# Optimization experiments

Hardware: AMD Instinct MI355X
Metric: run time of the kernel (lower is better)

Reference implementation:

```python
import jax, jax.numpy as jnp
import numpy as np

BN_EPS = 1e-5

def _bn_relu(x, gamma, beta, mean, var):
    # x: [B, N, C]; BatchNorm1d(N) in eval mode normalizes over dim=1 (N)
    inv = jax.lax.rsqrt(var + BN_EPS)
    scale = (gamma * inv)[None, :, None]
    shift = (beta - mean * gamma * inv)[None, :, None]
    return jax.nn.relu(x * scale + shift)

def _forward(x, q_gamma, q_beta, q_mean, q_var,
             k_gamma, k_beta, k_mean, k_var,
             v_gamma, v_beta, v_mean, v_var,
             Wq, Wk, Wv, Wp):
    B, C, H, W = x.shape
    N = H * W
    E = Wq.shape[0]
    xs = x.reshape(B, C, N).transpose(0, 2, 1)  # [B, N, C]
    # BN+ReLU over spatial axis, then Linear(N->E) on spatial axis per channel -> [B, E, C]
    q = jnp.einsum('bnc,en->bec', _bn_relu(xs, q_gamma, q_beta, q_mean, q_var), Wq)
    k = jnp.einsum('bnc,en->bec', _bn_relu(xs, k_gamma, k_beta, k_mean, k_var), Wk)
    v = jnp.einsum('bnc,en->bec', _bn_relu(xs, v_gamma, v_beta, v_mean, v_var), Wv)
    scores = jnp.einsum('bec,bfc->bef', q, k) / jnp.sqrt(jnp.asarray(E, x.dtype))  # [B, E, E]
    attn = jax.nn.softmax(scores, axis=-1)
    out = jnp.einsum('bef,bfc->bec', attn, v)          # [B, E, C]
    out = jnp.einsum('bec,ne->bcn', out, Wp)            # Linear(E->N) -> [B, C, N]
    return out.reshape(B, C, H, W)

def setup_inputs() -> dict:
    key = jax.random.key(0)
    ks = jax.random.split(key, 20)
    B, C, H, W = 32, 512, 32, 32
    N = H * W  # sp_dim = 1024
    E = 1024   # embed_dim
    d = {'x': jax.random.normal(ks[0], (B, C, H, W), jnp.float32)}
    i = 1
    for p in ('q', 'k', 'v'):
        d[f'{p}_gamma'] = jax.random.uniform(ks[i], (N,), jnp.float32, 0.5, 1.5); i += 1
        d[f'{p}_beta'] = 0.1 * jax.random.normal(ks[i], (N,), jnp.float32); i += 1
        d[f'{p}_mean'] = 0.1 * jax.random.normal(ks[i], (N,), jnp.float32); i += 1
        d[f'{p}_var'] = jax.random.uniform(ks[i], (N,), jnp.float32, 0.5, 1.5); i += 1
    # torch Linear weight layout: [out, in]; scale ~ 1/sqrt(fan_in)
    d['Wq'] = jax.random.normal(ks[i], (E, N), jnp.float32) * (1.0 / np.sqrt(N)); i += 1
    d['Wk'] = jax.random.normal(ks[i], (E, N), jnp.float32) * (1.0 / np.sqrt(N)); i += 1
    d['Wv'] = jax.random.normal(ks[i], (E, N), jnp.float32) * (1.0 / np.sqrt(N)); i += 1
    d['Wp'] = jax.random.normal(ks[i], (N, E), jnp.float32) * (1.0 / np.sqrt(E)); i += 1
    return d

def reference(x, q_gamma, q_beta, q_mean, q_var,
              k_gamma, k_beta, k_mean, k_var,
              v_gamma, v_beta, v_mean, v_var,
              Wq, Wk, Wv, Wp):
    return _forward(x, q_gamma, q_beta, q_mean, q_var,
                    k_gamma, k_beta, k_mean, k_var,
                    v_gamma, v_beta, v_mean, v_var,
                    Wq, Wk, Wv, Wp)
```

## Files before the change

### kernel.cpp

```cpp
#include <hip/hip_runtime.h>
#include <math.h>

#define BN_EPS 1e-5f

namespace {

constexpr int Bb = 32;
constexpr int Cc = 512;
constexpr int Nn = 1024;
constexpr int Ee = 1024;

typedef __attribute__((ext_vector_type(8))) short short8;
typedef __attribute__((ext_vector_type(4))) float f32x4;
typedef __attribute__((ext_vector_type(4))) unsigned short ushort4_t;

struct bfpair { unsigned short h, l; };

__device__ __forceinline__ unsigned short bf16_rne(float v) {
  unsigned u = __builtin_bit_cast(unsigned, v);
  unsigned r = u + 0x7FFFu + ((u >> 16) & 1u);
  return (unsigned short)(r >> 16);
}
__device__ __forceinline__ float bf16_to_f(unsigned short h) {
  unsigned u = ((unsigned)h) << 16;
  return __builtin_bit_cast(float, u);
}
__device__ __forceinline__ bfpair split_bf(float v) {
  bfpair p;
  p.h = bf16_rne(v);
  p.l = bf16_rne(v - bf16_to_f(p.h));
  return p;
}

__device__ __forceinline__ void gll16(const void* g, void* l) {
  __builtin_amdgcn_global_load_lds(
      (const __attribute__((address_space(1))) void*)g,
      (__attribute__((address_space(3))) void*)l, 16, 0, 0);
}

__global__ __launch_bounds__(256) void prep_st_kernel(
    const float* __restrict__ g, const float* __restrict__ be,
    const float* __restrict__ mn, const float* __restrict__ vr,
    float* __restrict__ s, float* __restrict__ t, int n) {
  int i = blockIdx.x * blockDim.x + threadIdx.x;
  if (i < n) {
    float inv = rsqrtf(vr[i] + BN_EPS);
    float sc = g[i] * inv;
    s[i] = sc;
    t[i] = be[i] - mn[i] * sc;
  }
}

__global__ __launch_bounds__(256) void convert_y(
    const float* __restrict__ x, const float* __restrict__ s, const float* __restrict__ tt,
    unsigned short* __restrict__ yh, unsigned short* __restrict__ yl, long total4) {
  for (long i = (long)blockIdx.x * 256 + threadIdx.x; i < total4; i += (long)gridDim.x * 256) {
    float4 v = ((const float4*)x)[i];
    int n4 = (int)(i & 255);
    float4 s4 = ((const float4*)s)[n4];
    float4 t4 = ((const float4*)tt)[n4];
    float e0 = fmaxf(fmaf(v.x, s4.x, t4.x), 0.f);
    float e1 = fmaxf(fmaf(v.y, s4.y, t4.y), 0.f);
    float e2 = fmaxf(fmaf(v.z, s4.z, t4.z), 0.f);
    float e3 = fmaxf(fmaf(v.w, s4.w, t4.w), 0.f);
    bfpair p0 = split_bf(e0), p1 = split_bf(e1), p2 = split_bf(e2), p3 = split_bf(e3);
    ushort4_t hv, lv;
    hv.x = p0.h; hv.y = p1.h; hv.z = p2.h; hv.w = p3.h;
    lv.x = p0.l; lv.y = p1.l; lv.z = p2.l; lv.w = p3.l;
    *(ushort4_t*)&yh[i * 4] = hv;
    *(ushort4_t*)&yl[i * 4] = lv;
  }
}

__global__ __launch_bounds__(256) void convert_w(
    const float* __restrict__ wsrc, unsigned short* __restrict__ wh,
    unsigned short* __restrict__ wl, long total4) {
  for (long i = (long)blockIdx.x * 256 + threadIdx.x; i < total4; i += (long)gridDim.x * 256) {
    float4 v = ((const float4*)wsrc)[i];
    bfpair p0 = split_bf(v.x), p1 = split_bf(v.y), p2 = split_bf(v.z), p3 = split_bf(v.w);
    ushort4_t hv, lv;
    hv.x = p0.h; hv.y = p1.h; hv.z = p2.h; hv.w = p3.h;
    lv.x = p0.l; lv.y = p1.l; lv.z = p2.l; lv.w = p3.l;
    *(ushort4_t*)&wh[i * 4] = hv;
    *(ushort4_t*)&wl[i * 4] = lv;
  }
}

template<bool SPLIT>
__global__ __launch_bounds__(256) void gemm3(
    const unsigned short* __restrict__ Ah, const unsigned short* __restrict__ Al,
    long ldA, long bsA,
    const unsigned short* __restrict__ Bh, const unsigned short* __restrict__ Bl,
    long ldB, long bsB,
    float* __restrict__ Cf, unsigned short* __restrict__ Chi, unsigned short* __restrict__ Clo,
    long ldC, long bsC, int K, float alpha) {
  __shared__ unsigned short sAh[128][32], sAl[128][32], sBh[128][32], sBl[128][32];

  const int t = threadIdx.x, lane = t & 63, w = t >> 6;
  const int m0 = blockIdx.y * 128, n0 = blockIdx.x * 128;
  const long zb = blockIdx.z;

  const int sr = lane >> 2;
  const int sk = (lane & 3) * 8;
  const int wr = w >> 1, wc = w & 1;
  const int fr = lane & 15;
  const int kq = (lane >> 4) * 8;

  const unsigned short* a0 = Ah + zb * bsA + (long)(m0 + w * 32 + sr) * ldA + sk;
  const unsigned short* a1 = Al + zb * bsA + (long)(m0 + w * 32 + sr) * ldA + sk;
  const unsigned short* b0 = Bh + zb * bsB + (long)(n0 + w * 32 + sr) * ldB + sk;
  const unsigned short* b1 = Bl + zb * bsB + (long)(n0 + w * 32 + sr) * ldB + sk;
  const long a16 = 16 * ldA, b16 = 16 * ldB;

  f32x4 acc[4][4] = {};

  for (int k0 = 0; k0 < K; k0 += 32) {
    __syncthreads();
    gll16(a0, &sAh[w * 32][0]);      gll16(a0 + a16, &sAh[w * 32 + 16][0]);
    gll16(a1, &sAl[w * 32][0]);      gll16(a1 + a16, &sAl[w * 32 + 16][0]);
    gll16(b0, &sBh[w * 32][0]);      gll16(b0 + b16, &sBh[w * 32 + 16][0]);
    gll16(b1, &sBl[w * 32][0]);      gll16(b1 + b16, &sBl[w * 32 + 16][0]);
    a0 += 32; a1 += 32; b0 += 32; b1 += 32;
    __syncthreads();

    short8 ah[4], al[4], bh[4], bl[4];
#pragma unroll
    for (int i = 0; i < 4; ++i) {
      ah[i] = *(const short8*)&sAh[wr * 64 + i * 16 + fr][kq];
      al[i] = *(const short8*)&sAl[wr * 64 + i * 16 + fr][kq];
      bh[i] = *(const short8*)&sBh[wc * 64 + i * 16 + fr][kq];
      bl[i] = *(const short8*)&sBl[wc * 64 + i * 16 + fr][kq];
    }
#pragma unroll
    for (int i = 0; i < 4; ++i)
#pragma unroll
      for (int j = 0; j < 4; ++j) {
        acc[i][j] = __builtin_amdgcn_mfma_f32_16x16x32_bf16(ah[i], bh[j], acc[i][j], 0, 0, 0);
        acc[i][j] = __builtin_amdgcn_mfma_f32_16x16x32_bf16(ah[i], bl[j], acc[i][j], 0, 0, 0);
        acc[i][j] = __builtin_amdgcn_mfma_f32_16x16x32_bf16(al[i], bh[j], acc[i][j], 0, 0, 0);
      }
  }

  const int rb = (lane >> 4) * 4;
#pragma unroll
  for (int i = 0; i < 4; ++i)
#pragma unroll
    for (int j = 0; j < 4; ++j) {
      long col = n0 + wc * 64 + j * 16 + fr;
#pragma unroll
      for (int v = 0; v < 4; ++v) {
        long row = m0 + wr * 64 + i * 16 + rb + v;
        float val = acc[i][j][v] * alpha;
        long idx = zb * bsC + row * ldC + col;
        if (SPLIT) {
          bfpair p = split_bf(val);
          Chi[idx] = p.h;
          Clo[idx] = p.l;
        } else {
          Cf[idx] = val;
        }
      }
    }
}

__global__ __launch_bounds__(256) void softmax_rows(float* __restrict__ S) {
  long row = blockIdx.x;
  float* p = S + row * 1024;
  int t = threadIdx.x;
  float4 v = *(float4*)(p + 4 * t);
  float mx = fmaxf(fmaxf(v.x, v.y), fmaxf(v.z, v.w));
#pragma unroll
  for (int i = 1; i < 64; i <<= 1) mx = fmaxf(mx, __shfl_xor(mx, i));
  __shared__ float redm[4];
  __shared__ float reds[4];
  int wave = t >> 6, lane = t & 63;
  if (lane == 0) redm[wave] = mx;
  __syncthreads();
  mx = fmaxf(fmaxf(redm[0], redm[1]), fmaxf(redm[2], redm[3]));
  float e0 = expf(v.x - mx), e1 = expf(v.y - mx);
  float e2 = expf(v.z - mx), e3 = expf(v.w - mx);
  float sum = (e0 + e1) + (e2 + e3);
#pragma unroll
  for (int i = 1; i < 64; i <<= 1) sum += __shfl_xor(sum, i);
  if (lane == 0) reds[wave] = sum;
  __syncthreads();
  sum = (reds[0] + reds[1]) + (reds[2] + reds[3]);
  float inv = 1.0f / sum;
  bfpair p0 = split_bf(e0 * inv), p1 = split_bf(e1 * inv);
  bfpair p2 = split_bf(e2 * inv), p3 = split_bf(e3 * inv);
  ushort4_t hv, lv;
  hv.x = p0.h; hv.y = p1.h; hv.z = p2.h; hv.w = p3.h;
  lv.x = p0.l; lv.y = p1.l; lv.z = p2.l; lv.w = p3.l;
  unsigned short* ph = (unsigned short*)p;
  *(ushort4_t*)&ph[4 * t] = hv;
  *(ushort4_t*)&ph[1024 + 4 * t] = lv;
}

}

extern "C" void kernel_launch(void* const* d_in, const int* in_sizes, int n_in,
                              void* d_out, int out_size, void* d_ws, size_t ws_size,
                              hipStream_t stream) {
  const float* x  = (const float*)d_in[0];
  const float* qg = (const float*)d_in[1];
  const float* qb = (const float*)d_in[2];
  const float* qm = (const float*)d_in[3];
  const float* qv = (const float*)d_in[4];
  const float* kg = (const float*)d_in[5];
  const float* kb = (const float*)d_in[6];
  const float* km = (const float*)d_in[7];
  const float* kv = (const float*)d_in[8];
  const float* vg = (const float*)d_in[9];
  const float* vb = (const float*)d_in[10];
  const float* vm = (const float*)d_in[11];
  const float* vv = (const float*)d_in[12];
  const float* Wq = (const float*)d_in[13];
  const float* Wk = (const float*)d_in[14];
  const float* Wv = (const float*)d_in[15];
  const float* Wp = (const float*)d_in[16];

  const size_t wMB = 8UL * 1024 * 1024 * 2;
  const size_t perB = 12UL * 1024 * 1024;
  int G = 32;
  while (G > 1 && 65536 + wMB + (size_t)G * perB > ws_size) G >>= 1;

  char* ws = (char*)d_ws;
  float* sq = (float*)ws;
  float* tq = sq + 1024;
  float* sk = tq + 1024;
  float* tk = sk + 1024;
  float* sv = tk + 1024;
  float* tv = sv + 1024;

  const long WE = 1024L * 1024;
  unsigned short* Wqh = (unsigned short*)(ws + 65536);
  unsigned short* Wql = Wqh + WE;
  unsigned short* Wkh = Wql + WE;
  unsigned short* Wkl = Wkh + WE;
  unsigned short* Wvh = Wkl + WE;
  unsigned short* Wvl = Wvh + WE;
  unsigned short* Wph = Wvl + WE;
  unsigned short* Wpl = Wph + WE;

  const long PB = (long)Cc * Ee;
  unsigned short* yh  = Wpl + WE;
  unsigned short* yl  = yh + (long)G * PB;
  unsigned short* Qh  = yl + (long)G * PB;
  unsigned short* Ql  = Qh + (long)G * PB;
  unsigned short* Kh  = Ql + (long)G * PB;
  unsigned short* Kl  = Kh + (long)G * PB;
  unsigned short* Vth = Kl + (long)G * PB;
  unsigned short* Vtl = Vth + (long)G * PB;
  float* S = (float*)(Vtl + (long)G * PB);
  unsigned short* Oth = Qh;
  unsigned short* Otl = Ql;

  dim3 blk(256);

  prep_st_kernel<<<dim3(4), blk, 0, stream>>>(qg, qb, qm, qv, sq, tq, Nn);
  prep_st_kernel<<<dim3(4), blk, 0, stream>>>(kg, kb, km, kv, sk, tk, Nn);
  prep_st_kernel<<<dim3(4), blk, 0, stream>>>(vg, vb, vm, vv, sv, tv, Nn);

  const long W4 = WE / 4;
  convert_w<<<dim3(1024), blk, 0, stream>>>(Wq, Wqh, Wql, W4);
  convert_w<<<dim3(1024), blk, 0, stream>>>(Wk, Wkh, Wkl, W4);
  convert_w<<<dim3(1024), blk, 0, stream>>>(Wv, Wvh, Wvl, W4);
  convert_w<<<dim3(1024), blk, 0, stream>>>(Wp, Wph, Wpl, W4);

  const long y4 = (long)G * PB / 4;

  for (int b0 = 0; b0 < Bb; b0 += G) {
    const float* xg = x + (size_t)b0 * Cc * Nn;
    float* outg = (float*)d_out + (size_t)b0 * Cc * Nn;

    convert_y<<<dim3(2048), blk, 0, stream>>>(xg, sq, tq, yh, yl, y4);
    gemm3<true><<<dim3(Cc / 128, Ee / 128, G), blk, 0, stream>>>(
        Wqh, Wql, Nn, 0L, yh, yl, Nn, PB,
        nullptr, Qh, Ql, Cc, PB, Nn, 1.0f);
    convert_y<<<dim3(2048), blk, 0, stream>>>(xg, sk, tk, yh, yl, y4);
    gemm3<true><<<dim3(Cc / 128, Ee / 128, G), blk, 0, stream>>>(
        Wkh, Wkl, Nn, 0L, yh, yl, Nn, PB,
        nullptr, Kh, Kl, Cc, PB, Nn, 1.0f);
    convert_y<<<dim3(2048), blk, 0, stream>>>(xg, sv, tv, yh, yl, y4);
    gemm3<true><<<dim3(Ee / 128, Cc / 128, G), blk, 0, stream>>>(
        yh, yl, Nn, PB, Wvh, Wvl, Nn, 0L,
        nullptr, Vth, Vtl, Ee, PB, Nn, 1.0f);
    gemm3<false><<<dim3(Ee / 128, Ee / 128, G), blk, 0, stream>>>(
        Qh, Ql, Cc, PB, Kh, Kl, Cc, PB,
        S, nullptr, nullptr, Ee, (long)Ee * Ee, Cc, 0.03125f);
    softmax_rows<<<dim3(G * Ee), blk, 0, stream>>>(S);
    gemm3<true><<<dim3(Ee / 128, Cc / 128, G), blk, 0, stream>>>(
        Vth, Vtl, Ee, PB, (unsigned short*)S, (unsigned short*)S + 1024,
        2L * Ee, 2L * Ee * Ee,
        nullptr, Oth, Otl, Ee, PB, Ee, 1.0f);
    gemm3<false><<<dim3(Nn / 128, Cc / 128, G), blk, 0, stream>>>(
        Oth, Otl, Ee, PB, Wph, Wpl, Ee, 0L,
        outg, nullptr, nullptr, Nn, (long)Cc * Nn, Ee, 1.0f);
  }
}
```

Before: 865.5 us.

## Fuse BN+ReLU+split into projection GEMMs, merge Q/K GEMM, swizzle LDS

Replaces the separate convert_y passes with a gemm_bn kernel that loads fp32 activations, applies BN+ReLU, splits them into bf16 hi/lo pairs and writes them straight to LDS inside the GEMM mainloop. Q and K projections are merged into one GEMM over a stacked 2048-row weight, and V is computed once for all batches into the output buffer as scratch. The change also adds XOR swizzling of LDS columns, a flattened 1D grid with block remapping, and fused prep of the three BN scale/shift vectors. The aim is to cut the intermediate bf16 activation traffic and launch count; in exchange the activation conversion is done with register loads in the GEMM, and the output buffer is reused for V, which relies on the P·V step reading each batch's V before the final projection overwrites it.

```diff
diff --git a/kernel.cpp b/kernel.cpp
--- a/kernel.cpp
+++ b/kernel.cpp
@@ -38,37 +38,23 @@
       (__attribute__((address_space(3))) void*)l, 16, 0, 0);
 }
 
-__global__ __launch_bounds__(256) void prep_st_kernel(
-    const float* __restrict__ g, const float* __restrict__ be,
-    const float* __restrict__ mn, const float* __restrict__ vr,
-    float* __restrict__ s, float* __restrict__ t, int n) {
+__global__ __launch_bounds__(256) void prep3(
+    const float* __restrict__ qg, const float* __restrict__ qb,
+    const float* __restrict__ qm, const float* __restrict__ qv,
+    const float* __restrict__ kg, const float* __restrict__ kb,
+    const float* __restrict__ km, const float* __restrict__ kv,
+    const float* __restrict__ vg, const float* __restrict__ vb,
+    const float* __restrict__ vm, const float* __restrict__ vv,
+    float* __restrict__ hdr) {
   int i = blockIdx.x * blockDim.x + threadIdx.x;
-  if (i < n) {
-    float inv = rsqrtf(vr[i] + BN_EPS);
-    float sc = g[i] * inv;
-    s[i] = sc;
-    t[i] = be[i] - mn[i] * sc;
-  }
-}
-
-__global__ __launch_bounds__(256) void convert_y(
-    const float* __restrict__ x, const float* __restrict__ s, const float* __restrict__ tt,
-    unsigned short* __restrict__ yh, unsigned short* __restrict__ yl, long total4) {
-  for (long i = (long)blockIdx.x * 256 + threadIdx.x; i < total4; i += (long)gridDim.x * 256) {
-    float4 v = ((const float4*)x)[i];
-    int n4 = (int)(i & 255);
-    float4 s4 = ((const float4*)s)[n4];
-    float4 t4 = ((const float4*)tt)[n4];
-    float e0 = fmaxf(fmaf(v.x, s4.x, t4.x), 0.f);
-    float e1 = fmaxf(fmaf(v.y, s4.y, t4.y), 0.f);
-    float e2 = fmaxf(fmaf(v.z, s4.z, t4.z), 0.f);
-    float e3 = fmaxf(fmaf(v.w, s4.w, t4.w), 0.f);
-    bfpair p0 = split_bf(e0), p1 = split_bf(e1), p2 = split_bf(e2), p3 = split_bf(e3);
-    ushort4_t hv, lv;
-    hv.x = p0.h; hv.y = p1.h; hv.z = p2.h; hv.w = p3.h;
-    lv.x = p0.l; lv.y = p1.l; lv.z = p2.l; lv.w = p3.l;
-    *(ushort4_t*)&yh[i * 4] = hv;
-    *(ushort4_t*)&yl[i * 4] = lv;
+  if (i < 1024) {
+    float inv, sc;
+    inv = rsqrtf(qv[i] + BN_EPS); sc = qg[i] * inv;
+    hdr[i] = sc;          hdr[1024 + i] = qb[i] - qm[i] * sc;
+    inv = rsqrtf(kv[i] + BN_EPS); sc = kg[i] * inv;
+    hdr[2048 + i] = sc;   hdr[3072 + i] = kb[i] - km[i] * sc;
+    inv = rsqrtf(vv[i] + BN_EPS); sc = vg[i] * inv;
+    hdr[4096 + i] = sc;   hdr[5120 + i] = vb[i] - vm[i] * sc;
   }
 }
 
@@ -86,6 +72,124 @@
   }
 }
 
+
+template<bool BN_ON_A, bool MFIRST>
+__global__ __launch_bounds__(256) void gemm_bn(
+    const unsigned short* __restrict__ Wh, const unsigned short* __restrict__ Wl,
+    const float* __restrict__ X, long bsX,
+    const float* __restrict__ s0, const float* __restrict__ t0,
+    const float* __restrict__ s1, const float* __restrict__ t1,
+    unsigned short* __restrict__ Chi, unsigned short* __restrict__ Clo,
+    long ldC, long bsC, int g0, int g1) {
+  constexpr int K = 1024;
+  __shared__ unsigned short sWh[128][32], sWl[128][32], sXh[128][32], sXl[128][32];
+
+  const int nb = gridDim.x;
+  int f = blockIdx.x;
+  if ((nb & 7) == 0) f = (f & 7) * (nb >> 3) + (f >> 3);
+  const int i0 = f % g0, i1 = (f / g0) % g1;
+  const long zb = f / (g0 * g1);
+  const int m0 = (MFIRST ? i0 : i1) * 128;
+  const int n0 = (MFIRST ? i1 : i0) * 128;
+
+  const int t = threadIdx.x, lane = t & 63, w = t >> 6;
+  const int sr  = lane >> 2;
+  const int skc = (((lane & 3) ^ ((lane >> 3) & 3)) * 8);
+  const int wr = w >> 1, wc = w & 1;
+  const int fr = lane & 15;
+  const int kq = ((((lane >> 4) & 3) ^ ((fr >> 1) & 3)) * 8);
+
+  const float* sb = s0;
+  const float* tb = t0;
+  if (!BN_ON_A && m0 >= 1024) { sb = s1; tb = t1; }
+
+  const int wrow0 = BN_ON_A ? n0 : m0;
+  const unsigned short* w0 = Wh + (long)(wrow0 + w * 32 + sr) * K + skc;
+  const unsigned short* w1 = Wl + (long)(wrow0 + w * 32 + sr) * K + skc;
+  const long w16 = 16L * K;
+
+  const int xrow0 = BN_ON_A ? m0 : n0;
+  const int xr = t >> 1, xh = t & 1;
+  const float* xp = X + zb * bsX + (long)(xrow0 + xr) * Nn + xh * 16;
+  const int swzr = (xr >> 1) & 3;
+
+  typedef unsigned short (*tile_t)[32];
+  tile_t pA0 = BN_ON_A ? sXh : sWh;
+  tile_t pA1 = BN_ON_A ? sXl : sWl;
+  tile_t pB0 = BN_ON_A ? sWh : sXh;
+  tile_t pB1 = BN_ON_A ? sWl : sXl;
+
+  f32x4 acc[4][4] = {};
+
+  for (int k0 = 0; k0 < K; k0 += 32) {
+    float4 xv[4];
+#pragma unroll
+    for (int j = 0; j < 4; ++j) xv[j] = *(const float4*)(xp + k0 + 4 * j);
+
+    __syncthreads();
+    gll16(w0, &sWh[w * 32][0]);  gll16(w0 + w16, &sWh[w * 32 + 16][0]);
+    gll16(w1, &sWl[w * 32][0]);  gll16(w1 + w16, &sWl[w * 32 + 16][0]);
+    w0 += 32; w1 += 32;
+
+    const int kbase = k0 + xh * 16;
+#pragma unroll
+    for (int cc = 0; cc < 2; ++cc) {
+      short8 hv, lv;
+#pragma unroll
+      for (int j = 0; j < 2; ++j) {
+        float4 v  = xv[cc * 2 + j];
+        float4 s4 = *(const float4*)(sb + kbase + cc * 8 + j * 4);
+        float4 t4 = *(const float4*)(tb + kbase + cc * 8 + j * 4);
+        bfpair p0 = split_bf(fmaxf(fmaf(v.x, s4.x, t4.x), 0.f));
+        bfpair p1 = split_bf(fmaxf(fmaf(v.y, s4.y, t4.y), 0.f));
+        bfpair p2 = split_bf(fmaxf(fmaf(v.z, s4.z, t4.z), 0.f));
+        bfpair p3 = split_bf(fmaxf(fmaf(v.w, s4.w, t4.w), 0.f));
+        hv[j * 4 + 0] = (short)p0.h; hv[j * 4 + 1] = (short)p1.h;
+        hv[j * 4 + 2] = (short)p2.h; hv[j * 4 + 3] = (short)p3.h;
+        lv[j * 4 + 0] = (short)p0.l; lv[j * 4 + 1] = (short)p1.l;
+        lv[j * 4 + 2] = (short)p2.l; lv[j * 4 + 3] = (short)p3.l;
+      }
+      const int swc = (xh * 2 + cc) ^ swzr;
+      *(short8*)&sXh[xr][swc * 8] = hv;
+      *(short8*)&sXl[xr][swc * 8] = lv;
+    }
+    __syncthreads();
+
+    short8 ah[4], al[4], bh[4], bl[4];
+#pragma unroll
+    for (int i = 0; i < 4; ++i) {
+      ah[i] = *(const short8*)&pA0[wr * 64 + i * 16 + fr][kq];
+      al[i] = *(const short8*)&pA1[wr * 64 + i * 16 + fr][kq];
+      bh[i] = *(const short8*)&pB0[wc * 64 + i * 16 + fr][kq];
+      bl[i] = *(const short8*)&pB1[wc * 64 + i * 16 + fr][kq];
+    }
+#pragma unroll
+    for (int i = 0; i < 4; ++i)
+#pragma unroll
+      for (int j = 0; j < 4; ++j) {
+        acc[i][j] = __builtin_amdgcn_mfma_f32_16x16x32_bf16(ah[i], bh[j], acc[i][j], 0, 0, 0);
+        acc[i][j] = __builtin_amdgcn_mfma_f32_16x16x32_bf16(ah[i], bl[j], acc[i][j], 0, 0, 0);
+        acc[i][j] = __builtin_amdgcn_mfma_f32_16x16x32_bf16(al[i], bh[j], acc[i][j], 0, 0, 0);
+      }
+  }
+
+  const int rb = ((lane >> 4) & 3) * 4;
+#pragma unroll
+  for (int i = 0; i < 4; ++i)
+#pragma unroll
+    for (int j = 0; j < 4; ++j) {
+      long col = n0 + wc * 64 + j * 16 + fr;
+#pragma unroll
+      for (int v = 0; v < 4; ++v) {
+        long row = m0 + wr * 64 + i * 16 + rb + v;
+        long idx = zb * bsC + row * ldC + col;
+        bfpair p = split_bf(acc[i][j][v]);
+        Chi[idx] = p.h;
+        Clo[idx] = p.l;
+      }
+    }
+}
+
 template<bool SPLIT>
 __global__ __launch_bounds__(256) void gemm3(
     const unsigned short* __restrict__ Ah, const unsigned short* __restrict__ Al,
@@ -93,23 +197,27 @@
     const unsigned short* __restrict__ Bh, const unsigned short* __restrict__ Bl,
     long ldB, long bsB,
     float* __restrict__ Cf, unsigned short* __restrict__ Chi, unsigned short* __restrict__ Clo,
-    long ldC, long bsC, int K, float alpha) {
+    long ldC, long bsC, int K, float alpha, int gx, int gy) {
   __shared__ unsigned short sAh[128][32], sAl[128][32], sBh[128][32], sBl[128][32];
 
+  const int nb = gridDim.x;
+  int f = blockIdx.x;
+  if ((nb & 7) == 0) f = (f & 7) * (nb >> 3) + (f >> 3);
+  const int n0 = (f % gx) * 128;
+  const int m0 = ((f / gx) % gy) * 128;
+  const long zb = f / (gx * gy);
+
   const int t = threadIdx.x, lane = t & 63, w = t >> 6;
-  const int m0 = blockIdx.y * 128, n0 = blockIdx.x * 128;
-  const long zb = blockIdx.z;
-
-  const int sr = lane >> 2;
-  const int sk = (lane & 3) * 8;
+  const int sr  = lane >> 2;
+  const int skc = (((lane & 3) ^ ((lane >> 3) & 3)) * 8);
   const int wr = w >> 1, wc = w & 1;
   const int fr = lane & 15;
-  const int kq = (lane >> 4) * 8;
-
-  const unsigned short* a0 = Ah + zb * bsA + (long)(m0 + w * 32 + sr) * ldA + sk;
-  const unsigned short* a1 = Al + zb * bsA + (long)(m0 + w * 32 + sr) * ldA + sk;
-  const unsigned short* b0 = Bh + zb * bsB + (long)(n0 + w * 32 + sr) * ldB + sk;
-  const unsigned short* b1 = Bl + zb * bsB + (long)(n0 + w * 32 + sr) * ldB + sk;
+  const int kq = ((((lane >> 4) & 3) ^ ((fr >> 1) & 3)) * 8);
+
+  const unsigned short* a0 = Ah + zb * bsA + (long)(m0 + w * 32 + sr) * ldA + skc;
+  const unsigned short* a1 = Al + zb * bsA + (long)(m0 + w * 32 + sr) * ldA + skc;
+  const unsigned short* b0 = Bh + zb * bsB + (long)(n0 + w * 32 + sr) * ldB + skc;
+  const unsigned short* b1 = Bl + zb * bsB + (long)(n0 + w * 32 + sr) * ldB + skc;
   const long a16 = 16 * ldA, b16 = 16 * ldB;
 
   f32x4 acc[4][4] = {};
@@ -141,7 +249,7 @@
       }
   }
 
-  const int rb = (lane >> 4) * 4;
+  const int rb = ((lane >> 4) & 3) * 4;
 #pragma unroll
   for (int i = 0; i < 4; ++i)
 #pragma unroll
@@ -219,82 +327,68 @@
   const float* Wv = (const float*)d_in[15];
   const float* Wp = (const float*)d_in[16];
 
-  const size_t wMB = 8UL * 1024 * 1024 * 2;
-  const size_t perB = 12UL * 1024 * 1024;
+  const size_t wFix = 65536 + 16UL * 1024 * 1024;
+  const size_t perB = 8UL * 1024 * 1024;
   int G = 32;
-  while (G > 1 && 65536 + wMB + (size_t)G * perB > ws_size) G >>= 1;
+  while (G > 1 && wFix + (size_t)G * perB > ws_size) G >>= 1;
 
   char* ws = (char*)d_ws;
-  float* sq = (float*)ws;
-  float* tq = sq + 1024;
-  float* sk = tq + 1024;
-  float* tk = sk + 1024;
-  float* sv = tk + 1024;
-  float* tv = sv + 1024;
+  float* hdr = (float*)ws;
+  float* sq = hdr;        float* tq = hdr + 1024;
+  float* sk = hdr + 2048; float* tk = hdr + 3072;
+  float* sv = hdr + 4096; float* tv = hdr + 5120;
 
   const long WE = 1024L * 1024;
-  unsigned short* Wqh = (unsigned short*)(ws + 65536);
-  unsigned short* Wql = Wqh + WE;
-  unsigned short* Wkh = Wql + WE;
-  unsigned short* Wkl = Wkh + WE;
-  unsigned short* Wvh = Wkl + WE;
-  unsigned short* Wvl = Wvh + WE;
-  unsigned short* Wph = Wvl + WE;
-  unsigned short* Wpl = Wph + WE;
-
-  const long PB = (long)Cc * Ee;
-  unsigned short* yh  = Wpl + WE;
-  unsigned short* yl  = yh + (long)G * PB;
-  unsigned short* Qh  = yl + (long)G * PB;
-  unsigned short* Ql  = Qh + (long)G * PB;
-  unsigned short* Kh  = Ql + (long)G * PB;
-  unsigned short* Kl  = Kh + (long)G * PB;
-  unsigned short* Vth = Kl + (long)G * PB;
-  unsigned short* Vtl = Vth + (long)G * PB;
-  float* S = (float*)(Vtl + (long)G * PB);
-  unsigned short* Oth = Qh;
-  unsigned short* Otl = Ql;
+  unsigned short* WQKh = (unsigned short*)(ws + 65536);
+  unsigned short* WQKl = WQKh + 2 * WE;
+  unsigned short* Wvh  = WQKl + 2 * WE;
+  unsigned short* Wvl  = Wvh + WE;
+  unsigned short* Wph  = Wvl + WE;
+  unsigned short* Wpl  = Wph + WE;
+
+  const long QKBS = 2048L * 512;
+  unsigned short* QKh = Wpl + WE;
+  unsigned short* QKl = QKh + (long)G * QKBS;
+  float* S = (float*)(QKl + (long)G * QKBS);
+
+  unsigned short* Vth = (unsigned short*)d_out;
+  const long VTBS = 1048576;
 
   dim3 blk(256);
 
-  prep_st_kernel<<<dim3(4), blk, 0, stream>>>(qg, qb, qm, qv, sq, tq, Nn);
-  prep_st_kernel<<<dim3(4), blk, 0, stream>>>(kg, kb, km, kv, sk, tk, Nn);
-  prep_st_kernel<<<dim3(4), blk, 0, stream>>>(vg, vb, vm, vv, sv, tv, Nn);
+  prep3<<<dim3(4), blk, 0, stream>>>(qg, qb, qm, qv, kg, kb, km, kv, vg, vb, vm, vv, hdr);
 
   const long W4 = WE / 4;
-  convert_w<<<dim3(1024), blk, 0, stream>>>(Wq, Wqh, Wql, W4);
-  convert_w<<<dim3(1024), blk, 0, stream>>>(Wk, Wkh, Wkl, W4);
+  convert_w<<<dim3(1024), blk, 0, stream>>>(Wq, WQKh, WQKl, W4);
+  convert_w<<<dim3(1024), blk, 0, stream>>>(Wk, WQKh + WE, WQKl + WE, W4);
   convert_w<<<dim3(1024), blk, 0, stream>>>(Wv, Wvh, Wvl, W4);
   convert_w<<<dim3(1024), blk, 0, stream>>>(Wp, Wph, Wpl, W4);
 
-  const long y4 = (long)G * PB / 4;
+  gemm_bn<true, false><<<dim3((Ee / 128) * (Cc / 128) * Bb), blk, 0, stream>>>(
+      Wvh, Wvl, x, (long)Cc * Nn, sv, tv, nullptr, nullptr,
+      Vth, Vth + 524288, Ee, VTBS, Ee / 128, Cc / 128);
 
   for (int b0 = 0; b0 < Bb; b0 += G) {
     const float* xg = x + (size_t)b0 * Cc * Nn;
-    float* outg = (float*)d_out + (size_t)b0 * Cc * Nn;
-
-    convert_y<<<dim3(2048), blk, 0, stream>>>(xg, sq, tq, yh, yl, y4);
-    gemm3<true><<<dim3(Cc / 128, Ee / 128, G), blk, 0, stream>>>(
-        Wqh, Wql, Nn, 0L, yh, yl, Nn, PB,
-        nullptr, Qh, Ql, Cc, PB, Nn, 1.0f);
-    convert_y<<<dim3(2048), blk, 0, stream>>>(xg, sk, tk, yh, yl, y4);
-    gemm3<true><<<dim3(Cc / 128, Ee / 128, G), blk, 0, stream>>>(
-        Wkh, Wkl, Nn, 0L, yh, yl, Nn, PB,
-        nullptr, Kh, Kl, Cc, PB, Nn, 1.0f);
-    convert_y<<<dim3(2048), blk, 0, stream>>>(xg, sv, tv, yh, yl, y4);
-    gemm3<true><<<dim3(Ee / 128, Cc / 128, G), blk, 0, stream>>>(
-        yh, yl, Nn, PB, Wvh, Wvl, Nn, 0L,
-        nullptr, Vth, Vtl, Ee, PB, Nn, 1.0f);
-    gemm3<false><<<dim3(Ee / 128, Ee / 128, G), blk, 0, stream>>>(
-        Qh, Ql, Cc, PB, Kh, Kl, Cc, PB,
-        S, nullptr, nullptr, Ee, (long)Ee * Ee, Cc, 0.03125f);
+
+    gemm_bn<false, true><<<dim3(16 * (Cc / 128) * G), blk, 0, stream>>>(
+        WQKh, WQKl, xg, (long)Cc * Nn, sq, tq, sk, tk,
+        QKh, QKl, Cc, QKBS, 16, Cc / 128);
+
+    gemm3<false><<<dim3((Ee / 128) * (Ee / 128) * G), blk, 0, stream>>>(
+        QKh, QKl, Cc, QKBS, QKh + 1024 * 512, QKl + 1024 * 512, Cc, QKBS,
+        S, nullptr, nullptr, Ee, 1048576L, Cc, 0.03125f, Ee / 128, Ee / 128);
+
     softmax_rows<<<dim3(G * Ee), blk, 0, stream>>>(S);
-    gemm3<true><<<dim3(Ee / 128, Cc / 128, G), blk, 0, stream>>>(
-        Vth, Vtl, Ee, PB, (unsigned short*)S, (unsigned short*)S + 1024,
-        2L * Ee, 2L * Ee * Ee,
-        nullptr, Oth, Otl, Ee, PB, Ee, 1.0f);
-    gemm3<false><<<dim3(Nn / 128, Cc / 128, G), blk, 0, stream>>>(
-        Oth, Otl, Ee, PB, Wph, Wpl, Ee, 0L,
-        outg, nullptr, nullptr, Nn, (long)Cc * Nn, Ee, 1.0f);
-  }
-}
+
+    gemm3<true><<<dim3((Ee / 128) * (Cc / 128) * G), blk, 0, stream>>>(
+        Vth + (long)b0 * VTBS, Vth + (long)b0 * VTBS + 524288, Ee, VTBS,
+        (unsigned short*)S, (unsigned short*)S + 1024, 2L * Ee, 2097152L,
+        nullptr, QKh, QKl, Ee, QKBS, Ee, 1.0f, Ee / 128, Cc / 128);
+
+    gemm3<false><<<dim3((Nn / 128) * (Cc / 128) * G), blk, 0, stream>>>(
+        QKh, QKl, Ee, QKBS, Wph, Wpl, Ee, 0L,
+        (float*)d_out + (size_t)b0 * Cc * Nn, nullptr, nullptr,
+        Nn, (long)Cc * Nn, Ee, 1.0f, Nn / 128, Cc / 128);
+  }
+}
```

New measurement: 853.5 us. Within noise of the previous version (-1.4%).
